# Kernel tuning notes

Measured on AMD Instinct MI355X. Metric: run time of the kernel, lower is better.

Reference implementation:

```python
import jax, jax.numpy as jnp
import numpy as np

B, S, H = 8, 1024, 1024
NH, HD = 16, 64
MBANK, TOPK = 128, 16
NLAYERS, FF = 12, 4096
EPS = 1e-5


def _ln(x, w, b):
    m = x.mean(-1, keepdims=True)
    v = ((x - m) ** 2).mean(-1, keepdims=True)
    return (x - m) / jnp.sqrt(v + EPS) * w + b


def _split_heads(x):  # [B,S,H] -> [B,NH,S,HD]
    return x.reshape(B, S, NH, HD).transpose(0, 2, 1, 3)


def _sdpa(q, k, v):  # inputs [B,NH,S,HD]
    scores = jnp.einsum('bhqd,bhkd->bhqk', q, k) / jnp.sqrt(jnp.float32(HD))
    attn = jax.nn.softmax(scores, axis=-1)
    o = jnp.einsum('bhqk,bhkd->bhqd', attn, v)
    return o.transpose(0, 2, 1, 3).reshape(B, S, H)


def setup_inputs() -> dict:
    key = jax.random.key(0)
    ks = jax.random.split(key, 24)
    n = lambda k, shp, s=0.02: jax.random.normal(k, shp, jnp.float32) * s
    return {
        'hidden_states': jax.random.normal(ks[0], (B, S, H), jnp.float32),
        'ln1_w': jnp.ones((H,), jnp.float32), 'ln1_b': jnp.zeros((H,), jnp.float32),
        'ln2_w': jnp.ones((H,), jnp.float32), 'ln2_b': jnp.zeros((H,), jnp.float32),
        'rec_wq': n(ks[1], (H, H)), 'rec_wk': n(ks[2], (H, H)),
        'rec_wv': n(ks[3], (H, H)), 'rec_wo': n(ks[4], (H, H)),
        'rec_ad_w1': n(ks[5], (H // 4, H)), 'rec_ad_w2': n(ks[6], (H, H // 4)),
        'mem_bank': n(ks[7], (MBANK, H)),
        'alloc_w': n(ks[8], (MBANK, H)), 'alloc_b': jnp.zeros((MBANK,), jnp.float32),
        'retr_w': n(ks[9], (MBANK, H)), 'retr_b': jnp.zeros((MBANK,), jnp.float32),
        'upd_w': n(ks[10], (H, H)), 'upd_b': jnp.zeros((H,), jnp.float32),
        'mem_scales': jnp.full((NLAYERS,), 0.1, jnp.float32),
        'attn_in_w': n(ks[11], (3 * H, H)), 'attn_in_b': jnp.zeros((3 * H,), jnp.float32),
        'attn_out_w': n(ks[12], (H, H)), 'attn_out_b': jnp.zeros((H,), jnp.float32),
        'mlp_w1': n(ks[13], (FF, H)), 'mlp_b1': jnp.zeros((FF,), jnp.float32),
        'mlp_w2': n(ks[14], (H, FF)), 'mlp_b2': jnp.zeros((H,), jnp.float32),
        'layer_idx': 4,
    }


def reference(hidden_states, ln1_w, ln1_b, ln2_w, ln2_b,
              rec_wq, rec_wk, rec_wv, rec_wo, rec_ad_w1, rec_ad_w2,
              mem_bank, alloc_w, alloc_b, retr_w, retr_b, upd_w, upd_b, mem_scales,
              attn_in_w, attn_in_b, attn_out_w, attn_out_b,
              mlp_w1, mlp_b1, mlp_w2, mlp_b2, layer_idx):
    residual = hidden_states
    h = _ln(hidden_states, ln1_w, ln1_b)

    # --- CrossLayerParameterRecycler (layer_idx % 4 == 0 and > 0 -> recycle) ---
    if layer_idx % 4 == 0 and layer_idx > 0:
        q = _split_heads(h @ rec_wq.T)
        k = _split_heads(h @ rec_wk.T)
        v = _split_heads(h @ rec_wv.T)
        base_out = _sdpa(q, k, v) @ rec_wo.T
        h = jax.nn.relu(base_out @ rec_ad_w1.T) @ rec_ad_w2.T

    # --- CrossLayerMemoryManager ---
    pooled = h.mean(axis=1)                                  # [B,H]
    alloc_weights = jax.nn.softmax(pooled @ alloc_w.T + alloc_b, axis=-1)   # [B,MBANK]
    retr_weights = jax.nn.softmax(pooled @ retr_w.T + retr_b, axis=-1)
    retrieved = retr_weights @ mem_bank                      # [B,H]
    h = h + retrieved[:, None, :] * mem_scales[layer_idx]
    update_signals = jax.nn.sigmoid(h.mean(axis=1) @ upd_w.T + upd_b)       # [B,H]
    _, top_idx = jax.lax.top_k(alloc_weights, TOPK)          # [B,TOPK]

    # sequential per-batch scatter (later batches overwrite earlier, as in torch loop)
    def _write(mb, be):
        idx, sig = be
        return mb.at[idx].set(jnp.broadcast_to(sig, (TOPK, H))), None
    new_mem_bank, _ = jax.lax.scan(_write, mem_bank, (top_idx, update_signals))

    # --- self attention (nn.MultiheadAttention, batch_first) ---
    qkv = h @ attn_in_w.T + attn_in_b                        # [B,S,3H]
    q, k, v = jnp.split(qkv, 3, axis=-1)
    attn_out = _sdpa(_split_heads(q), _split_heads(k), _split_heads(v))
    attn_out = attn_out @ attn_out_w.T + attn_out_b
    h = residual + attn_out

    # --- MLP block ---
    residual2 = h
    h = _ln(h, ln2_w, ln2_b)
    h = jax.nn.gelu(h @ mlp_w1.T + mlp_b1, approximate=False) @ mlp_w2.T + mlp_b2
    out = residual2 + h
    return out, new_mem_bank
```

## Files before the change

kernel.cpp:

```cpp
#include <hip/hip_runtime.h>
#include <hip/hip_bf16.h>
#include <math.h>
#include <stdint.h>


#define BB 8
#define SS 1024
#define HH 1024
#define NHEAD 16
#define HD 64
#define MBANK 128
#define TOPK_N 16
#define FF_DIM 4096
#define MROWS (BB * SS)
#define NB_ELEM (8ull*1024*1024)

typedef __bf16 bf16x8 __attribute__((ext_vector_type(8)));
typedef __bf16 bf16x4 __attribute__((ext_vector_type(4)));
typedef float f32x4 __attribute__((ext_vector_type(4)));

#define SCALE_LOG2E 0.18033688011112042f

__device__ __forceinline__ unsigned short f2b(float x) {
  unsigned u = __float_as_uint(x);
  unsigned r = (u + 0x7FFFu + ((u >> 16) & 1u)) >> 16;
  return (unsigned short)r;
}
__device__ __forceinline__ float b2f(unsigned short u) {
  return __uint_as_float((unsigned)u << 16);
}

__device__ __forceinline__ float hmax4(f32x4 v) {
  return fmaxf(fmaxf(v[0], v[1]), fmaxf(v[2], v[3]));
}

__device__ __forceinline__ void load16_lds(const void* g, void* lds_base, int lane) {
#if __has_builtin(__builtin_amdgcn_global_load_lds)
  typedef const __attribute__((address_space(1))) unsigned int guint;
  typedef __attribute__((address_space(3))) unsigned int luint;
  __builtin_amdgcn_global_load_lds((guint*)(uintptr_t)g,
                                   (luint*)(unsigned long long)(unsigned int)(uintptr_t)lds_base,
                                   16, 0, 0);
#else
  *(uint4*)((char*)lds_base + lane * 16) = *(const uint4*)g;
#endif
}

__device__ __forceinline__ float gelu_exact(float x) {
  return 0.5f * x * (1.f + erff(x * 0.70710678118654752440f));
}


__global__ __launch_bounds__(256) void cast_split(const float* __restrict__ s,
                                                  unsigned short* __restrict__ hi,
                                                  unsigned short* __restrict__ lo, int n4) {
  int i = blockIdx.x * 256 + threadIdx.x;
  if (i < n4) {
    float4 v = ((const float4*)s)[i];
    ushort4 h, l;
    h.x = f2b(v.x); l.x = f2b(v.x - b2f(h.x));
    h.y = f2b(v.y); l.y = f2b(v.y - b2f(h.y));
    h.z = f2b(v.z); l.z = f2b(v.z - b2f(h.z));
    h.w = f2b(v.w); l.w = f2b(v.w - b2f(h.w));
    ((ushort4*)hi)[i] = h;
    ((ushort4*)lo)[i] = l;
  }
}

__global__ __launch_bounds__(256) void ln3(const float* __restrict__ x,
                                           const float* __restrict__ w,
                                           const float* __restrict__ b,
                                           unsigned short* __restrict__ yh,
                                           unsigned short* __restrict__ yl) {
  int row = blockIdx.x;
  const float* xr = x + (size_t)row * HH;
  int t = threadIdx.x;
  float v[4];
  float s = 0.f, ss = 0.f;
#pragma unroll
  for (int i = 0; i < 4; i++) {
    v[i] = xr[t + i * 256];
    s += v[i];
    ss += v[i] * v[i];
  }
  __shared__ float rs[8], rss[8];
  for (int o = 32; o > 0; o >>= 1) {
    s += __shfl_down(s, o, 64);
    ss += __shfl_down(ss, o, 64);
  }
  int wid = t >> 6, lane = t & 63;
  if (lane == 0) { rs[wid] = s; rss[wid] = ss; }
  __syncthreads();
  if (t == 0) {
    float S = rs[0] + rs[1] + rs[2] + rs[3];
    float SSum = rss[0] + rss[1] + rss[2] + rss[3];
    float m = S * (1.f / HH);
    float var = SSum * (1.f / HH) - m * m;
    rs[4] = m;
    rs[5] = rsqrtf(var + 1e-5f);
  }
  __syncthreads();
  float m = rs[4], inv = rs[5];
#pragma unroll
  for (int i = 0; i < 4; i++) {
    int c = t + i * 256;
    float y = (v[i] - m) * inv * w[c] + b[c];
    unsigned short h = f2b(y);
    yh[(size_t)row * HH + c] = h;
    yl[(size_t)row * HH + c] = f2b(y - b2f(h));
  }
}

template <int ACT, int MODE>
__global__ __launch_bounds__(256) void gemm3(const unsigned short* __restrict__ Ah,
                                             const unsigned short* __restrict__ Al, int lda,
                                             const unsigned short* __restrict__ Wh,
                                             const unsigned short* __restrict__ Wl, int ldw,
                                             unsigned short* __restrict__ Oh,
                                             unsigned short* __restrict__ Ol,
                                             float* __restrict__ outF,
                                             int ldo, int K) {
  __shared__ unsigned short Ash[2][128 * 32];
  __shared__ unsigned short Asl[2][128 * 32];
  __shared__ unsigned short Bsh[2][128 * 32];
  __shared__ unsigned short Bsl[2][128 * 32];
  int n0 = blockIdx.x * 128, m0 = blockIdx.y * 128;
  int t = threadIdx.x, w = t >> 6, L = t & 63, quad = L >> 4, l16 = L & 15;
  int wm = w & 1, wn = w >> 1;
  const f32x4 vzero = {0.f, 0.f, 0.f, 0.f};
  f32x4 acc[4][4];
#pragma unroll
  for (int i = 0; i < 4; i++)
#pragma unroll
    for (int j = 0; j < 4; j++) acc[i][j] = vzero;
  int srow = L >> 2;
  int scol = ((L & 3) ^ ((L >> 3) & 3)) * 8;
  int rsw = (l16 >> 1) & 3;

  auto stage = [&](int buf, int k0) {
#pragma unroll
    for (int c = 0; c < 2; c++) {
      int r = (c * 4 + w) * 16 + srow;
      size_t aoff = (size_t)(m0 + r) * lda + k0 + scol;
      size_t boff = (size_t)(n0 + r) * ldw + k0 + scol;
      load16_lds(Ah + aoff, &Ash[buf][(c * 4 + w) * 512], L);
      load16_lds(Al + aoff, &Asl[buf][(c * 4 + w) * 512], L);
      load16_lds(Wh + boff, &Bsh[buf][(c * 4 + w) * 512], L);
      load16_lds(Wl + boff, &Bsl[buf][(c * 4 + w) * 512], L);
    }
  };
  auto compute = [&](int buf) {
    bf16x8 afh[4], afl[4], bfh[4], bfl[4];
#pragma unroll
    for (int i = 0; i < 4; i++) {
      int off = (wm * 64 + i * 16 + l16) * 32 + (quad ^ rsw) * 8;
      afh[i] = *(const bf16x8*)&Ash[buf][off];
      afl[i] = *(const bf16x8*)&Asl[buf][off];
    }
#pragma unroll
    for (int j = 0; j < 4; j++) {
      int off = (wn * 64 + j * 16 + l16) * 32 + (quad ^ rsw) * 8;
      bfh[j] = *(const bf16x8*)&Bsh[buf][off];
      bfl[j] = *(const bf16x8*)&Bsl[buf][off];
    }
#pragma unroll
    for (int i = 0; i < 4; i++)
#pragma unroll
      for (int j = 0; j < 4; j++) {
        acc[i][j] = __builtin_amdgcn_mfma_f32_16x16x32_bf16(afh[i], bfh[j], acc[i][j], 0, 0, 0);
        acc[i][j] = __builtin_amdgcn_mfma_f32_16x16x32_bf16(afh[i], bfl[j], acc[i][j], 0, 0, 0);
        acc[i][j] = __builtin_amdgcn_mfma_f32_16x16x32_bf16(afl[i], bfh[j], acc[i][j], 0, 0, 0);
      }
  };

  stage(0, 0);
  __syncthreads();
  for (int k0 = 0; k0 < K; k0 += 64) {
    stage(1, k0 + 32);
    compute(0);
    __syncthreads();
    if (k0 + 64 < K) stage(0, k0 + 64);
    compute(1);
    __syncthreads();
  }
#pragma unroll
  for (int i = 0; i < 4; i++) {
    int mb = m0 + wm * 64 + i * 16 + quad * 4;
#pragma unroll
    for (int j = 0; j < 4; j++) {
      int n = n0 + wn * 64 + j * 16 + l16;
      if (MODE == 1) {
        ushort4 sh, sl;
        float vv[4];
#pragma unroll
        for (int r = 0; r < 4; r++) {
          float v = acc[i][j][r];
          if (ACT == 1) v = fmaxf(v, 0.f);
          vv[r] = v;
        }
        sh.x = f2b(vv[0]); sl.x = f2b(vv[0] - b2f(sh.x));
        sh.y = f2b(vv[1]); sl.y = f2b(vv[1] - b2f(sh.y));
        sh.z = f2b(vv[2]); sl.z = f2b(vv[2] - b2f(sh.z));
        sh.w = f2b(vv[3]); sl.w = f2b(vv[3] - b2f(sh.w));
        *(ushort4*)&Oh[(size_t)n * ldo + mb] = sh;
        *(ushort4*)&Ol[(size_t)n * ldo + mb] = sl;
      } else {
#pragma unroll
        for (int r = 0; r < 4; r++) {
          float v = acc[i][j][r];
          if (ACT == 1) v = fmaxf(v, 0.f);
          size_t off = (size_t)(mb + r) * ldo + n;
          if (MODE == 0) {
            unsigned short h = f2b(v);
            Oh[off] = h;
            Ol[off] = f2b(v - b2f(h));
          } else {
            outF[off] = v;
          }
        }
      }
    }
  }
}

__global__ __launch_bounds__(256) void sdpa3(const unsigned short* __restrict__ Qh,
                                             const unsigned short* __restrict__ Ql,
                                             const unsigned short* __restrict__ Kh,
                                             const unsigned short* __restrict__ Kl,
                                             const unsigned short* __restrict__ Vth,
                                             const unsigned short* __restrict__ Vtl,
                                             unsigned short* __restrict__ Oh,
                                             unsigned short* __restrict__ Ol) {
  __shared__ unsigned short Ksh[64 * 64];
  __shared__ unsigned short Ksl[64 * 64];
  __shared__ unsigned short Vsh[64 * 64];
  __shared__ unsigned short Vsl[64 * 64];
  int qt = blockIdx.x, h = blockIdx.y, b = blockIdx.z;
  int t = threadIdx.x, w = t >> 6, L = t & 63, quad = L >> 4, l16 = L & 15;
  int q0 = qt * 64;
  const f32x4 vzero = {0.f, 0.f, 0.f, 0.f};
  bf16x8 qfh[2], qfl[2];
  {
    size_t qrow = (size_t)(b * SS + q0 + w * 16 + l16);
#pragma unroll
    for (int kh = 0; kh < 2; kh++) {
      size_t off = qrow * HH + h * 64 + kh * 32 + quad * 8;
      qfh[kh] = *(const bf16x8*)&Qh[off];
      qfl[kh] = *(const bf16x8*)&Ql[off];
    }
  }
  float mprev = -1e30f, lsum = 0.f;
  f32x4 oacc[4];
#pragma unroll
  for (int jd = 0; jd < 4; jd++) oacc[jd] = vzero;
  int srow = L >> 3;
  int scolV = ((L & 7) ^ srow) * 8;
  int rbase = ((l16 & 12) << 1) | (l16 & 3);
  int keyK = (l16 & 3) | (((l16 >> 2) & 1) << 2);
  int k7 = l16 & 7;
  for (int k0 = 0; k0 < SS; k0 += 64) {
    __syncthreads();
#pragma unroll
    for (int c = 0; c < 2; c++) {
      int rr = (c * 4 + w) * 8 + srow;
      int scolK = ((L & 7) ^ ((srow & 3) | (((c * 4 + w) & 1) << 2))) * 8;
      size_t koff = (size_t)(b * SS + k0 + rr) * HH + h * 64 + scolK;
      size_t voff = (size_t)(h * 64 + rr) * MROWS + b * SS + k0 + scolV;
      load16_lds(Kh + koff, &Ksh[(c * 4 + w) * 512], L);
      load16_lds(Kl + koff, &Ksl[(c * 4 + w) * 512], L);
      load16_lds(Vth + voff, &Vsh[(c * 4 + w) * 512], L);
      load16_lds(Vtl + voff, &Vsl[(c * 4 + w) * 512], L);
    }
    __syncthreads();
    f32x4 sacc[4];
#pragma unroll
    for (int jn = 0; jn < 4; jn++) sacc[jn] = vzero;
#pragma unroll
    for (int jn = 0; jn < 4; jn++) {
      int rowp = rbase + (jn & 1) * 4 + (jn >> 1) * 32;
#pragma unroll
      for (int kh = 0; kh < 2; kh++) {
        int off = rowp * 64 + (((kh * 4 + quad) ^ keyK) << 3);
        bf16x8 kfh = *(const bf16x8*)&Ksh[off];
        bf16x8 kfl = *(const bf16x8*)&Ksl[off];
        sacc[jn] = __builtin_amdgcn_mfma_f32_16x16x32_bf16(kfh, qfh[kh], sacc[jn], 0, 0, 0);
        sacc[jn] = __builtin_amdgcn_mfma_f32_16x16x32_bf16(kfl, qfh[kh], sacc[jn], 0, 0, 0);
        sacc[jn] = __builtin_amdgcn_mfma_f32_16x16x32_bf16(kfh, qfl[kh], sacc[jn], 0, 0, 0);
      }
    }
    float mt = fmaxf(fmaxf(hmax4(sacc[0]), hmax4(sacc[1])),
                     fmaxf(hmax4(sacc[2]), hmax4(sacc[3])));
    mt = fmaxf(mt, __shfl_xor(mt, 16, 64));
    mt = fmaxf(mt, __shfl_xor(mt, 32, 64));
    float m2 = fmaxf(mprev, mt * SCALE_LOG2E);
    float alpha = exp2f(mprev - m2);
    mprev = m2;
    float rs = 0.f;
    bf16x8 pah[2], pal[2];
#pragma unroll
    for (int jn = 0; jn < 4; jn++) {
      int kh = jn >> 1, half = (jn & 1) * 4;
#pragma unroll
      for (int r = 0; r < 4; r++) {
        float p = exp2f(fmaf(sacc[jn][r], SCALE_LOG2E, -m2));
        rs += p;
        __bf16 ph = (__bf16)p;
        pah[kh][half + r] = ph;
        pal[kh][half + r] = (__bf16)(p - (float)ph);
      }
    }
    rs += __shfl_xor(rs, 16, 64);
    rs += __shfl_xor(rs, 32, 64);
    lsum = lsum * alpha + rs;
    float ar[4];
#pragma unroll
    for (int r = 0; r < 4; r++) ar[r] = __shfl(alpha, quad * 4 + r, 16);
#pragma unroll
    for (int jd = 0; jd < 4; jd++)
#pragma unroll
      for (int r = 0; r < 4; r++) oacc[jd][r] *= ar[r];
#pragma unroll
    for (int jd = 0; jd < 4; jd++)
#pragma unroll
      for (int kh = 0; kh < 2; kh++) {
        int off = (jd * 16 + l16) * 64 + ((kh * 4 + quad) ^ k7) * 8;
        bf16x8 vfh = *(const bf16x8*)&Vsh[off];
        bf16x8 vfl = *(const bf16x8*)&Vsl[off];
        oacc[jd] = __builtin_amdgcn_mfma_f32_16x16x32_bf16(pah[kh], vfh, oacc[jd], 0, 0, 0);
        oacc[jd] = __builtin_amdgcn_mfma_f32_16x16x32_bf16(pah[kh], vfl, oacc[jd], 0, 0, 0);
        oacc[jd] = __builtin_amdgcn_mfma_f32_16x16x32_bf16(pal[kh], vfh, oacc[jd], 0, 0, 0);
      }
  }
  float inv = 1.f / lsum;
  float invr[4];
#pragma unroll
  for (int r = 0; r < 4; r++) invr[r] = __shfl(inv, quad * 4 + r, 16);
#pragma unroll
  for (int r = 0; r < 4; r++) {
    size_t row = (size_t)(b * SS + q0 + w * 16 + quad * 4 + r);
#pragma unroll
    for (int jd = 0; jd < 4; jd++) {
      float v = oacc[jd][r] * invr[r];
      unsigned short hh = f2b(v);
      size_t off = row * HH + h * 64 + jd * 16 + l16;
      Oh[off] = hh;
      Ol[off] = f2b(v - b2f(hh));
    }
  }
}


__global__ __launch_bounds__(256) void meanpool_kernel(const float* __restrict__ Hb,
                                                       float* __restrict__ P) {
  int cb = blockIdx.x;
  int b = blockIdx.y;
  int t = threadIdx.x;
  int c = (t & 63) + cb * 64;
  int part = t >> 6;
  float s = 0.f;
  const float* p = Hb + ((size_t)b * SS + part * 256) * HH + c;
  for (int j = 0; j < 256; j++) s += p[(size_t)j * HH];
  __shared__ float red[4][64];
  red[part][t & 63] = s;
  __syncthreads();
  if (t < 64) {
    float tot = red[0][t] + red[1][t] + red[2][t] + red[3][t];
    P[b * HH + cb * 64 + t] = tot * (1.f / SS);
  }
}

__global__ __launch_bounds__(256) void memlogits_kernel(const float* __restrict__ P,
                                                        const float* __restrict__ AW,
                                                        const float* __restrict__ ABias,
                                                        const float* __restrict__ RW,
                                                        const float* __restrict__ RBias,
                                                        float* __restrict__ LA,
                                                        float* __restrict__ LR) {
  int m = blockIdx.x, b = blockIdx.y;
  int t = threadIdx.x;
  const float* pr = P + b * HH;
  const float* aw = AW + (size_t)m * HH;
  const float* rw = RW + (size_t)m * HH;
  float sa = 0.f, sr = 0.f;
  for (int i = t; i < HH; i += 256) {
    float pv = pr[i];
    sa = fmaf(pv, aw[i], sa);
    sr = fmaf(pv, rw[i], sr);
  }
  for (int o = 32; o > 0; o >>= 1) {
    sa += __shfl_down(sa, o, 64);
    sr += __shfl_down(sr, o, 64);
  }
  __shared__ float ra[4], rr[4];
  if ((t & 63) == 0) { ra[t >> 6] = sa; rr[t >> 6] = sr; }
  __syncthreads();
  if (t == 0) {
    LA[b * MBANK + m] = ra[0] + ra[1] + ra[2] + ra[3] + ABias[m];
    LR[b * MBANK + m] = rr[0] + rr[1] + rr[2] + rr[3] + RBias[m];
  }
}

__global__ __launch_bounds__(256) void retrieve_kernel(const float* __restrict__ LA,
                                                       const float* __restrict__ LR,
                                                       const float* __restrict__ MB,
                                                       float* __restrict__ RET,
                                                       int* __restrict__ ISTOP) {
  int b = blockIdx.x;
  int t = threadIdx.x;
  __shared__ float rw[MBANK];
  __shared__ float la[MBANK];
  if (t < MBANK) {
    la[t] = LA[b * MBANK + t];
    rw[t] = LR[b * MBANK + t];
  }
  __syncthreads();
  if (t == 0) {
    float mx = -1e30f;
    for (int i = 0; i < MBANK; i++) mx = fmaxf(mx, rw[i]);
    float s = 0.f;
    for (int i = 0; i < MBANK; i++) {
      float e = __expf(rw[i] - mx);
      rw[i] = e;
      s += e;
    }
    float inv = 1.f / s;
    for (int i = 0; i < MBANK; i++) rw[i] *= inv;
  }
  __syncthreads();
  if (t < MBANK) {
    float mine = la[t];
    int rank = 0;
    for (int i = 0; i < MBANK; i++) {
      float o = la[i];
      if (o > mine || (o == mine && i < t)) rank++;
    }
    ISTOP[b * MBANK + t] = (rank < TOPK_N) ? 1 : 0;
  }
  for (int c = t; c < HH; c += 256) {
    float s = 0.f;
    for (int m = 0; m < MBANK; m++) s = fmaf(rw[m], MB[(size_t)m * HH + c], s);
    RET[b * HH + c] = s;
  }
}

__global__ __launch_bounds__(256) void addmem_kernel(float* __restrict__ Hb,
                                                     const float* __restrict__ RET,
                                                     const float* __restrict__ scales,
                                                     const int* __restrict__ lidx) {
  float sc = scales[lidx[0]];
  size_t i = (size_t)blockIdx.x * 256 + threadIdx.x;
  int c = (int)(i & 1023);
  int b = (int)(i >> 20);
  Hb[i] = fmaf(RET[b * HH + c], sc, Hb[i]);
}

__global__ __launch_bounds__(256) void upd_kernel(const float* __restrict__ P2,
                                                  const float* __restrict__ UW,
                                                  const float* __restrict__ UB,
                                                  float* __restrict__ UPD) {
  int n = blockIdx.x, b = blockIdx.y;
  int t = threadIdx.x;
  const float* pr = P2 + b * HH;
  const float* wr = UW + (size_t)n * HH;
  float s = 0.f;
  for (int i = t; i < HH; i += 256) s = fmaf(pr[i], wr[i], s);
  for (int o = 32; o > 0; o >>= 1) s += __shfl_down(s, o, 64);
  __shared__ float red[4];
  if ((t & 63) == 0) red[t >> 6] = s;
  __syncthreads();
  if (t == 0) {
    float tot = red[0] + red[1] + red[2] + red[3] + UB[n];
    UPD[b * HH + n] = 1.f / (1.f + __expf(-tot));
  }
}

__global__ __launch_bounds__(256) void membank_kernel(const float* __restrict__ MB,
                                                      const int* __restrict__ ISTOP,
                                                      const float* __restrict__ UPD,
                                                      float* __restrict__ OUT) {
  int row = blockIdx.x;
  int col = blockIdx.y * 256 + threadIdx.x;
  int w = -1;
  for (int b = 0; b < BB; b++)
    if (ISTOP[b * MBANK + row]) w = b;
  float v = (w >= 0) ? UPD[w * HH + col] : MB[(size_t)row * HH + col];
  OUT[(size_t)row * HH + col] = v;
}


__global__ __launch_bounds__(256) void ln_bf(const float* __restrict__ x,
                                             const float* __restrict__ w,
                                             const float* __restrict__ b,
                                             unsigned short* __restrict__ y) {
  int row = blockIdx.x;
  const float* xr = x + (size_t)row * HH;
  unsigned short* yr = y + (size_t)row * HH;
  int t = threadIdx.x;
  float v[4];
  float s = 0.f, ss = 0.f;
#pragma unroll
  for (int i = 0; i < 4; i++) {
    v[i] = xr[t + i * 256];
    s += v[i];
    ss += v[i] * v[i];
  }
  __shared__ float rs[8], rss[8];
  for (int o = 32; o > 0; o >>= 1) {
    s += __shfl_down(s, o, 64);
    ss += __shfl_down(ss, o, 64);
  }
  int wid = t >> 6, lane = t & 63;
  if (lane == 0) { rs[wid] = s; rss[wid] = ss; }
  __syncthreads();
  if (t == 0) {
    float S = rs[0] + rs[1] + rs[2] + rs[3];
    float SSum = rss[0] + rss[1] + rss[2] + rss[3];
    float m = S * (1.f / HH);
    float var = SSum * (1.f / HH) - m * m;
    rs[4] = m;
    rs[5] = rsqrtf(var + 1e-5f);
  }
  __syncthreads();
  float m = rs[4], inv = rs[5];
#pragma unroll
  for (int i = 0; i < 4; i++) {
    int c = t + i * 256;
    yr[c] = f2b((v[i] - m) * inv * w[c] + b[c]);
  }
}

__global__ __launch_bounds__(256) void castf2b(const float* __restrict__ s,
                                               unsigned short* __restrict__ d, int n4) {
  int i = blockIdx.x * 256 + threadIdx.x;
  if (i < n4) {
    float4 v = ((const float4*)s)[i];
    ushort4 o;
    o.x = f2b(v.x); o.y = f2b(v.y); o.z = f2b(v.z); o.w = f2b(v.w);
    ((ushort4*)d)[i] = o;
  }
}

template <int ACT, int MODE>
__global__ __launch_bounds__(256) void gemm_bf(const unsigned short* __restrict__ A, int lda,
                                               const unsigned short* __restrict__ W, int ldw,
                                               const float* __restrict__ bias,
                                               const float* __restrict__ resid,
                                               float* __restrict__ outF,
                                               unsigned short* __restrict__ outB,
                                               int ldo, int K) {
  __shared__ unsigned short As[2][128 * 32];
  __shared__ unsigned short Bs[2][128 * 32];
  int n0 = blockIdx.x * 128, m0 = blockIdx.y * 128;
  int t = threadIdx.x, w = t >> 6, L = t & 63, quad = L >> 4, l16 = L & 15;
  int wm = w & 1, wn = w >> 1;
  const f32x4 vzero = {0.f, 0.f, 0.f, 0.f};
  f32x4 acc[4][4];
#pragma unroll
  for (int i = 0; i < 4; i++)
#pragma unroll
    for (int j = 0; j < 4; j++) acc[i][j] = vzero;
  int srow = L >> 2;
  int scol = ((L & 3) ^ ((L >> 3) & 3)) * 8;
  int rsw = (l16 >> 1) & 3;

  auto stage = [&](int buf, int k0) {
#pragma unroll
    for (int c = 0; c < 2; c++) {
      int r = (c * 4 + w) * 16 + srow;
      load16_lds(A + (size_t)(m0 + r) * lda + k0 + scol, &As[buf][(c * 4 + w) * 512], L);
      load16_lds(W + (size_t)(n0 + r) * ldw + k0 + scol, &Bs[buf][(c * 4 + w) * 512], L);
    }
  };
  auto compute = [&](int buf) {
    bf16x8 af[4], bfr[4];
#pragma unroll
    for (int i = 0; i < 4; i++)
      af[i] = *(const bf16x8*)&As[buf][(wm * 64 + i * 16 + l16) * 32 + (quad ^ rsw) * 8];
#pragma unroll
    for (int j = 0; j < 4; j++)
      bfr[j] = *(const bf16x8*)&Bs[buf][(wn * 64 + j * 16 + l16) * 32 + (quad ^ rsw) * 8];
#pragma unroll
    for (int i = 0; i < 4; i++)
#pragma unroll
      for (int j = 0; j < 4; j++)
        acc[i][j] = __builtin_amdgcn_mfma_f32_16x16x32_bf16(af[i], bfr[j], acc[i][j], 0, 0, 0);
  };

  stage(0, 0);
  __syncthreads();
  for (int k0 = 0; k0 < K; k0 += 64) {
    stage(1, k0 + 32);
    compute(0);
    __syncthreads();
    if (k0 + 64 < K) stage(0, k0 + 64);
    compute(1);
    __syncthreads();
  }
#pragma unroll
  for (int i = 0; i < 4; i++) {
    int mb = m0 + wm * 64 + i * 16 + quad * 4;
#pragma unroll
    for (int j = 0; j < 4; j++) {
      int n = n0 + wn * 64 + j * 16 + l16;
      float bv = bias ? bias[n] : 0.f;
      if (MODE == 2) {
        ushort4 st;
        float v0 = acc[i][j][0] + bv, v1 = acc[i][j][1] + bv;
        float v2 = acc[i][j][2] + bv, v3 = acc[i][j][3] + bv;
        if (ACT == 1) { v0 = fmaxf(v0, 0.f); v1 = fmaxf(v1, 0.f); v2 = fmaxf(v2, 0.f); v3 = fmaxf(v3, 0.f); }
        if (ACT == 2) { v0 = gelu_exact(v0); v1 = gelu_exact(v1); v2 = gelu_exact(v2); v3 = gelu_exact(v3); }
        st.x = f2b(v0); st.y = f2b(v1); st.z = f2b(v2); st.w = f2b(v3);
        *(ushort4*)&outB[(size_t)n * ldo + mb] = st;
      } else {
#pragma unroll
        for (int r = 0; r < 4; r++) {
          float v = acc[i][j][r] + bv;
          if (ACT == 1) v = fmaxf(v, 0.f);
          if (ACT == 2) v = gelu_exact(v);
          size_t off = (size_t)(mb + r) * ldo + n;
          if (MODE == 1) outB[off] = f2b(v);
          else if (MODE == 3) outF[off] += v;
          else if (MODE == 4) outF[off] = v + resid[off];
        }
      }
    }
  }
}

__global__ __launch_bounds__(256) void sdpa_bf(const unsigned short* __restrict__ Q,
                                               const unsigned short* __restrict__ Kb,
                                               const unsigned short* __restrict__ Vt,
                                               unsigned short* __restrict__ O) {
  __shared__ unsigned short Ks[64 * 64];
  __shared__ unsigned short Vs[64 * 64];
  int qt = blockIdx.x, h = blockIdx.y, b = blockIdx.z;
  int t = threadIdx.x, w = t >> 6, L = t & 63, quad = L >> 4, l16 = L & 15;
  int q0 = qt * 64;
  const f32x4 vzero = {0.f, 0.f, 0.f, 0.f};
  bf16x8 qf[2];
  {
    size_t qrow = (size_t)(b * SS + q0 + w * 16 + l16);
#pragma unroll
    for (int kh = 0; kh < 2; kh++)
      qf[kh] = *(const bf16x8*)&Q[qrow * HH + h * 64 + kh * 32 + quad * 8];
  }
  float mprev = -1e30f, lsum = 0.f;
  f32x4 oacc[4];
#pragma unroll
  for (int jd = 0; jd < 4; jd++) oacc[jd] = vzero;
  int srow = L >> 3;
  int scolV = ((L & 7) ^ srow) * 8;
  int rbase = ((l16 & 12) << 1) | (l16 & 3);
  int keyK = (l16 & 3) | (((l16 >> 2) & 1) << 2);
  int k7 = l16 & 7;
  for (int k0 = 0; k0 < SS; k0 += 64) {
    __syncthreads();
#pragma unroll
    for (int c = 0; c < 2; c++) {
      int rr = (c * 4 + w) * 8 + srow;
      int scolK = ((L & 7) ^ ((srow & 3) | (((c * 4 + w) & 1) << 2))) * 8;
      load16_lds(Kb + (size_t)(b * SS + k0 + rr) * HH + h * 64 + scolK, &Ks[(c * 4 + w) * 512], L);
      load16_lds(Vt + (size_t)(h * 64 + rr) * MROWS + b * SS + k0 + scolV, &Vs[(c * 4 + w) * 512], L);
    }
    __syncthreads();
    f32x4 sacc[4];
#pragma unroll
    for (int jn = 0; jn < 4; jn++) sacc[jn] = vzero;
#pragma unroll
    for (int jn = 0; jn < 4; jn++) {
      int rowp = rbase + (jn & 1) * 4 + (jn >> 1) * 32;
#pragma unroll
      for (int kh = 0; kh < 2; kh++) {
        bf16x8 kf = *(const bf16x8*)&Ks[rowp * 64 + (((kh * 4 + quad) ^ keyK) << 3)];
        sacc[jn] = __builtin_amdgcn_mfma_f32_16x16x32_bf16(kf, qf[kh], sacc[jn], 0, 0, 0);
      }
    }
    float mt = fmaxf(fmaxf(hmax4(sacc[0]), hmax4(sacc[1])),
                     fmaxf(hmax4(sacc[2]), hmax4(sacc[3])));
    mt = fmaxf(mt, __shfl_xor(mt, 16, 64));
    mt = fmaxf(mt, __shfl_xor(mt, 32, 64));
    float m2 = fmaxf(mprev, mt * SCALE_LOG2E);
    float alpha = exp2f(mprev - m2);
    mprev = m2;
    float rs = 0.f;
    bf16x8 pa[2];
#pragma unroll
    for (int jn = 0; jn < 4; jn++) {
      int kh = jn >> 1, half = (jn & 1) * 4;
#pragma unroll
      for (int r = 0; r < 4; r++) {
        float p = exp2f(fmaf(sacc[jn][r], SCALE_LOG2E, -m2));
        rs += p;
        pa[kh][half + r] = (__bf16)p;
      }
    }
    rs += __shfl_xor(rs, 16, 64);
    rs += __shfl_xor(rs, 32, 64);
    lsum = lsum * alpha + rs;
    float ar[4];
#pragma unroll
    for (int r = 0; r < 4; r++) ar[r] = __shfl(alpha, quad * 4 + r, 16);
#pragma unroll
    for (int jd = 0; jd < 4; jd++)
#pragma unroll
      for (int r = 0; r < 4; r++) oacc[jd][r] *= ar[r];
#pragma unroll
    for (int jd = 0; jd < 4; jd++)
#pragma unroll
      for (int kh = 0; kh < 2; kh++) {
        bf16x8 vf = *(const bf16x8*)&Vs[(jd * 16 + l16) * 64 + ((kh * 4 + quad) ^ k7) * 8];
        oacc[jd] = __builtin_amdgcn_mfma_f32_16x16x32_bf16(pa[kh], vf, oacc[jd], 0, 0, 0);
      }
  }
  float inv = 1.f / lsum;
  float invr[4];
#pragma unroll
  for (int r = 0; r < 4; r++) invr[r] = __shfl(inv, quad * 4 + r, 16);
#pragma unroll
  for (int r = 0; r < 4; r++) {
    size_t row = (size_t)(b * SS + q0 + w * 16 + quad * 4 + r);
#pragma unroll
    for (int jd = 0; jd < 4; jd++)
      O[row * HH + h * 64 + jd * 16 + l16] = f2b(oacc[jd][r] * invr[r]);
  }
}

extern "C" void kernel_launch(void* const* d_in, const int* in_sizes, int n_in,
                              void* d_out, int out_size, void* d_ws, size_t ws_size,
                              hipStream_t stream) {
  const float* x = (const float*)d_in[0];
  const float* ln1_w = (const float*)d_in[1];
  const float* ln1_b = (const float*)d_in[2];
  const float* ln2_w = (const float*)d_in[3];
  const float* ln2_b = (const float*)d_in[4];
  const float* rec_wq = (const float*)d_in[5];
  const float* rec_wk = (const float*)d_in[6];
  const float* rec_wv = (const float*)d_in[7];
  const float* rec_wo = (const float*)d_in[8];
  const float* rec_ad_w1 = (const float*)d_in[9];
  const float* rec_ad_w2 = (const float*)d_in[10];
  const float* mem_bank = (const float*)d_in[11];
  const float* alloc_w = (const float*)d_in[12];
  const float* alloc_b = (const float*)d_in[13];
  const float* retr_w = (const float*)d_in[14];
  const float* retr_b = (const float*)d_in[15];
  const float* upd_w = (const float*)d_in[16];
  const float* upd_b = (const float*)d_in[17];
  const float* mem_scales = (const float*)d_in[18];
  const float* attn_in_w = (const float*)d_in[19];
  const float* attn_in_b = (const float*)d_in[20];
  const float* attn_out_w = (const float*)d_in[21];
  const float* attn_out_b = (const float*)d_in[22];
  const float* mlp_w1 = (const float*)d_in[23];
  const float* mlp_b1 = (const float*)d_in[24];
  const float* mlp_w2 = (const float*)d_in[25];
  const float* mlp_b2 = (const float*)d_in[26];
  const int* layer_idx = (const int*)d_in[27];

  float* out = (float*)d_out;
  float* out_mb = out + NB_ELEM;

  const size_t U = NB_ELEM;
  unsigned short* W16 = (unsigned short*)d_ws;
  unsigned short* U0 = W16;
  unsigned short* U1 = W16 + U;
  unsigned short* U2 = W16 + 2 * U;
  unsigned short* U3 = W16 + 3 * U;
  unsigned short* U4 = W16 + 4 * U;
  unsigned short* U5 = W16 + 5 * U;
  unsigned short* wsh = W16 + 6 * U;
  unsigned short* wsl = wsh + 1048576;
  float* small = (float*)(wsl + 1048576);
  float* pooled = small;
  float* pooled2 = small + 8192;
  float* logitsA = small + 16384;
  float* logitsR = small + 17408;
  float* retrieved = small + 18432;
  float* updsig = small + 26624;
  int* istop = (int*)(small + 34816);
  unsigned short* D0 = (unsigned short*)out;
  unsigned short* D1 = D0 + U;
  unsigned short* ain_bf = U5;
  unsigned short* aout_bf = U5 + 3 * 1048576;

  dim3 blk(256);
  dim3 gG(8, 64);
  dim3 gG256(2, 64);
  dim3 gS(16, NHEAD, BB);
  const int EW_GRID = (int)(NB_ELEM / 256);

  ln3<<<MROWS, blk, 0, stream>>>(x, ln1_w, ln1_b, U0, U1);
  cast_split<<<1024, blk, 0, stream>>>(rec_wq, wsh, wsl, 262144);
  gemm3<0, 0><<<gG, blk, 0, stream>>>(U0, U1, HH, wsh, wsl, HH, U2, U3, nullptr, HH, HH);
  cast_split<<<1024, blk, 0, stream>>>(rec_wk, wsh, wsl, 262144);
  gemm3<0, 0><<<gG, blk, 0, stream>>>(U0, U1, HH, wsh, wsl, HH, U4, U5, nullptr, HH, HH);
  cast_split<<<1024, blk, 0, stream>>>(rec_wv, wsh, wsl, 262144);
  gemm3<0, 1><<<gG, blk, 0, stream>>>(U0, U1, HH, wsh, wsl, HH, D0, D1, nullptr, MROWS, HH);
  sdpa3<<<gS, blk, 0, stream>>>(U2, U3, U4, U5, D0, D1, U0, U1);
  cast_split<<<1024, blk, 0, stream>>>(rec_wo, wsh, wsl, 262144);
  gemm3<0, 0><<<gG, blk, 0, stream>>>(U0, U1, HH, wsh, wsl, HH, U2, U3, nullptr, HH, HH);
  cast_split<<<256, blk, 0, stream>>>(rec_ad_w1, wsh, wsl, 65536);
  gemm3<1, 0><<<gG256, blk, 0, stream>>>(U2, U3, HH, wsh, wsl, HH, U4, U4 + 2097152, nullptr, 256, HH);
  cast_split<<<256, blk, 0, stream>>>(rec_ad_w2, wsh, wsl, 65536);
  gemm3<0, 2><<<gG, blk, 0, stream>>>(U4, U4 + 2097152, 256, wsh, wsl, 256, nullptr, nullptr, out, HH, 256);
  meanpool_kernel<<<dim3(HH / 64, BB), blk, 0, stream>>>(out, pooled);
  memlogits_kernel<<<dim3(MBANK, BB), blk, 0, stream>>>(pooled, alloc_w, alloc_b, retr_w, retr_b, logitsA, logitsR);
  retrieve_kernel<<<BB, blk, 0, stream>>>(logitsA, logitsR, mem_bank, retrieved, istop);
  addmem_kernel<<<EW_GRID, blk, 0, stream>>>(out, retrieved, mem_scales, layer_idx);
  meanpool_kernel<<<dim3(HH / 64, BB), blk, 0, stream>>>(out, pooled2);
  upd_kernel<<<dim3(HH, BB), blk, 0, stream>>>(pooled2, upd_w, upd_b, updsig);
  membank_kernel<<<dim3(MBANK, HH / 256), blk, 0, stream>>>(mem_bank, istop, updsig, out_mb);
  castf2b<<<8192, blk, 0, stream>>>(out, U0, 2097152);
  castf2b<<<3072, blk, 0, stream>>>(attn_in_w, ain_bf, 786432);
  castf2b<<<1024, blk, 0, stream>>>(attn_out_w, aout_bf, 262144);
  gemm_bf<0, 1><<<gG, blk, 0, stream>>>(U0, HH, ain_bf, HH, attn_in_b, nullptr, nullptr, U1, HH, HH);
  gemm_bf<0, 1><<<gG, blk, 0, stream>>>(U0, HH, ain_bf + (size_t)HH * HH, HH, attn_in_b + HH, nullptr, nullptr, U2, HH, HH);
  gemm_bf<0, 2><<<gG, blk, 0, stream>>>(U0, HH, ain_bf + 2ull * HH * HH, HH, attn_in_b + 2 * HH, nullptr, nullptr, U3, MROWS, HH);
  sdpa_bf<<<gS, blk, 0, stream>>>(U1, U2, U3, U4);
  gemm_bf<0, 4><<<gG, blk, 0, stream>>>(U4, HH, aout_bf, HH, attn_out_b, x, out, nullptr, HH, HH);
  ln_bf<<<MROWS, blk, 0, stream>>>(out, ln2_w, ln2_b, U1);
  {
    unsigned short* w1b = U0;
    unsigned short* w2b = U0 + 4 * 1048576;
    unsigned short* h2 = U2;
    castf2b<<<4096, blk, 0, stream>>>(mlp_w1, w1b, 1048576);
    castf2b<<<4096, blk, 0, stream>>>(mlp_w2, w2b, 1048576);
    gemm_bf<2, 1><<<dim3(32, 64), blk, 0, stream>>>(U1, HH, w1b, HH, mlp_b1, nullptr, nullptr, h2, FF_DIM, HH);
    gemm_bf<0, 3><<<gG, blk, 0, stream>>>(h2, FF_DIM, w2b, FF_DIM, mlp_b2, nullptr, out, nullptr, HH, FF_DIM);
  }
}
```

Measured before the change: 1.136 ms.

## Double-buffer K/V tiles, swizzle block order, skip redundant rescale in attention

Both attention kernels now keep two K/V buffers in LDS and load the next 64-key tile while computing on the current one, halving the barriers per tile. The grid becomes 1-D, and the block index is remapped so blocks that run at the same time spread across XCDs while sharing batch and head data. The online-softmax rescale of the accumulator is skipped when no lane's running max changed. LDS use per block doubles, which may reduce occupancy, and the wave-level branch adds a small divergence check.

```diff
diff --git a/kernel.cpp b/kernel.cpp
--- a/kernel.cpp
+++ b/kernel.cpp
@@ -231,11 +231,13 @@
                                              const unsigned short* __restrict__ Vtl,
                                              unsigned short* __restrict__ Oh,
                                              unsigned short* __restrict__ Ol) {
-  __shared__ unsigned short Ksh[64 * 64];
-  __shared__ unsigned short Ksl[64 * 64];
-  __shared__ unsigned short Vsh[64 * 64];
-  __shared__ unsigned short Vsl[64 * 64];
-  int qt = blockIdx.x, h = blockIdx.y, b = blockIdx.z;
+  __shared__ unsigned short Ksh[2][64 * 64];
+  __shared__ unsigned short Ksl[2][64 * 64];
+  __shared__ unsigned short Vsh[2][64 * 64];
+  __shared__ unsigned short Vsl[2][64 * 64];
+  int wg = (int)blockIdx.x;
+  int swz = (wg & 7) * 256 + (wg >> 3);
+  int qt = swz & 15, h = (swz >> 4) & 15, b = swz >> 8;
   int t = threadIdx.x, w = t >> 6, L = t & 63, quad = L >> 4, l16 = L & 15;
   int q0 = qt * 64;
   const f32x4 vzero = {0.f, 0.f, 0.f, 0.f};
@@ -258,20 +260,22 @@
   int rbase = ((l16 & 12) << 1) | (l16 & 3);
   int keyK = (l16 & 3) | (((l16 >> 2) & 1) << 2);
   int k7 = l16 & 7;
-  for (int k0 = 0; k0 < SS; k0 += 64) {
-    __syncthreads();
+
+  auto stage = [&](int buf, int k0) {
 #pragma unroll
     for (int c = 0; c < 2; c++) {
       int rr = (c * 4 + w) * 8 + srow;
       int scolK = ((L & 7) ^ ((srow & 3) | (((c * 4 + w) & 1) << 2))) * 8;
       size_t koff = (size_t)(b * SS + k0 + rr) * HH + h * 64 + scolK;
       size_t voff = (size_t)(h * 64 + rr) * MROWS + b * SS + k0 + scolV;
-      load16_lds(Kh + koff, &Ksh[(c * 4 + w) * 512], L);
-      load16_lds(Kl + koff, &Ksl[(c * 4 + w) * 512], L);
-      load16_lds(Vth + voff, &Vsh[(c * 4 + w) * 512], L);
-      load16_lds(Vtl + voff, &Vsl[(c * 4 + w) * 512], L);
-    }
-    __syncthreads();
+      load16_lds(Kh + koff, &Ksh[buf][(c * 4 + w) * 512], L);
+      load16_lds(Kl + koff, &Ksl[buf][(c * 4 + w) * 512], L);
+      load16_lds(Vth + voff, &Vsh[buf][(c * 4 + w) * 512], L);
+      load16_lds(Vtl + voff, &Vsl[buf][(c * 4 + w) * 512], L);
+    }
+  };
+
+  auto computeTile = [&](int buf) {
     f32x4 sacc[4];
 #pragma unroll
     for (int jn = 0; jn < 4; jn++) sacc[jn] = vzero;
@@ -281,8 +285,8 @@
 #pragma unroll
       for (int kh = 0; kh < 2; kh++) {
         int off = rowp * 64 + (((kh * 4 + quad) ^ keyK) << 3);
-        bf16x8 kfh = *(const bf16x8*)&Ksh[off];
-        bf16x8 kfl = *(const bf16x8*)&Ksl[off];
+        bf16x8 kfh = *(const bf16x8*)&Ksh[buf][off];
+        bf16x8 kfl = *(const bf16x8*)&Ksl[buf][off];
         sacc[jn] = __builtin_amdgcn_mfma_f32_16x16x32_bf16(kfh, qfh[kh], sacc[jn], 0, 0, 0);
         sacc[jn] = __builtin_amdgcn_mfma_f32_16x16x32_bf16(kfl, qfh[kh], sacc[jn], 0, 0, 0);
         sacc[jn] = __builtin_amdgcn_mfma_f32_16x16x32_bf16(kfh, qfl[kh], sacc[jn], 0, 0, 0);
@@ -293,8 +297,6 @@
     mt = fmaxf(mt, __shfl_xor(mt, 16, 64));
     mt = fmaxf(mt, __shfl_xor(mt, 32, 64));
     float m2 = fmaxf(mprev, mt * SCALE_LOG2E);
-    float alpha = exp2f(mprev - m2);
-    mprev = m2;
     float rs = 0.f;
     bf16x8 pah[2], pal[2];
 #pragma unroll
@@ -311,25 +313,42 @@
     }
     rs += __shfl_xor(rs, 16, 64);
     rs += __shfl_xor(rs, 32, 64);
-    lsum = lsum * alpha + rs;
-    float ar[4];
-#pragma unroll
-    for (int r = 0; r < 4; r++) ar[r] = __shfl(alpha, quad * 4 + r, 16);
-#pragma unroll
-    for (int jd = 0; jd < 4; jd++)
-#pragma unroll
-      for (int r = 0; r < 4; r++) oacc[jd][r] *= ar[r];
+    if (__any(m2 != mprev)) {
+      float alpha = exp2f(mprev - m2);
+      lsum = lsum * alpha + rs;
+      float ar[4];
+#pragma unroll
+      for (int r = 0; r < 4; r++) ar[r] = __shfl(alpha, quad * 4 + r, 16);
+#pragma unroll
+      for (int jd = 0; jd < 4; jd++)
+#pragma unroll
+        for (int r = 0; r < 4; r++) oacc[jd][r] *= ar[r];
+    } else {
+      lsum += rs;
+    }
+    mprev = m2;
 #pragma unroll
     for (int jd = 0; jd < 4; jd++)
 #pragma unroll
       for (int kh = 0; kh < 2; kh++) {
         int off = (jd * 16 + l16) * 64 + ((kh * 4 + quad) ^ k7) * 8;
-        bf16x8 vfh = *(const bf16x8*)&Vsh[off];
-        bf16x8 vfl = *(const bf16x8*)&Vsl[off];
+        bf16x8 vfh = *(const bf16x8*)&Vsh[buf][off];
+        bf16x8 vfl = *(const bf16x8*)&Vsl[buf][off];
         oacc[jd] = __builtin_amdgcn_mfma_f32_16x16x32_bf16(pah[kh], vfh, oacc[jd], 0, 0, 0);
         oacc[jd] = __builtin_amdgcn_mfma_f32_16x16x32_bf16(pah[kh], vfl, oacc[jd], 0, 0, 0);
         oacc[jd] = __builtin_amdgcn_mfma_f32_16x16x32_bf16(pal[kh], vfh, oacc[jd], 0, 0, 0);
       }
+  };
+
+  stage(0, 0);
+  __syncthreads();
+  for (int k0 = 0; k0 < SS; k0 += 128) {
+    stage(1, k0 + 64);
+    computeTile(0);
+    __syncthreads();
+    if (k0 + 128 < SS) stage(0, k0 + 128);
+    computeTile(1);
+    __syncthreads();
   }
   float inv = 1.f / lsum;
   float invr[4];
@@ -631,9 +650,11 @@
                                                const unsigned short* __restrict__ Kb,
                                                const unsigned short* __restrict__ Vt,
                                                unsigned short* __restrict__ O) {
-  __shared__ unsigned short Ks[64 * 64];
-  __shared__ unsigned short Vs[64 * 64];
-  int qt = blockIdx.x, h = blockIdx.y, b = blockIdx.z;
+  __shared__ unsigned short Ks[2][64 * 64];
+  __shared__ unsigned short Vs[2][64 * 64];
+  int wg = (int)blockIdx.x;
+  int swz = (wg & 7) * 256 + (wg >> 3);
+  int qt = swz & 15, h = (swz >> 4) & 15, b = swz >> 8;
   int t = threadIdx.x, w = t >> 6, L = t & 63, quad = L >> 4, l16 = L & 15;
   int q0 = qt * 64;
   const f32x4 vzero = {0.f, 0.f, 0.f, 0.f};
@@ -653,16 +674,18 @@
   int rbase = ((l16 & 12) << 1) | (l16 & 3);
   int keyK = (l16 & 3) | (((l16 >> 2) & 1) << 2);
   int k7 = l16 & 7;
-  for (int k0 = 0; k0 < SS; k0 += 64) {
-    __syncthreads();
+
+  auto stage = [&](int buf, int k0) {
 #pragma unroll
     for (int c = 0; c < 2; c++) {
       int rr = (c * 4 + w) * 8 + srow;
       int scolK = ((L & 7) ^ ((srow & 3) | (((c * 4 + w) & 1) << 2))) * 8;
-      load16_lds(Kb + (size_t)(b * SS + k0 + rr) * HH + h * 64 + scolK, &Ks[(c * 4 + w) * 512], L);
-      load16_lds(Vt + (size_t)(h * 64 + rr) * MROWS + b * SS + k0 + scolV, &Vs[(c * 4 + w) * 512], L);
-    }
-    __syncthreads();
+      load16_lds(Kb + (size_t)(b * SS + k0 + rr) * HH + h * 64 + scolK, &Ks[buf][(c * 4 + w) * 512], L);
+      load16_lds(Vt + (size_t)(h * 64 + rr) * MROWS + b * SS + k0 + scolV, &Vs[buf][(c * 4 + w) * 512], L);
+    }
+  };
+
+  auto computeTile = [&](int buf) {
     f32x4 sacc[4];
 #pragma unroll
     for (int jn = 0; jn < 4; jn++) sacc[jn] = vzero;
@@ -671,7 +694,7 @@
       int rowp = rbase + (jn & 1) * 4 + (jn >> 1) * 32;
 #pragma unroll
       for (int kh = 0; kh < 2; kh++) {
-        bf16x8 kf = *(const bf16x8*)&Ks[rowp * 64 + (((kh * 4 + quad) ^ keyK) << 3)];
+        bf16x8 kf = *(const bf16x8*)&Ks[buf][rowp * 64 + (((kh * 4 + quad) ^ keyK) << 3)];
         sacc[jn] = __builtin_amdgcn_mfma_f32_16x16x32_bf16(kf, qf[kh], sacc[jn], 0, 0, 0);
       }
     }
@@ -680,8 +703,6 @@
     mt = fmaxf(mt, __shfl_xor(mt, 16, 64));
     mt = fmaxf(mt, __shfl_xor(mt, 32, 64));
     float m2 = fmaxf(mprev, mt * SCALE_LOG2E);
-    float alpha = exp2f(mprev - m2);
-    mprev = m2;
     float rs = 0.f;
     bf16x8 pa[2];
 #pragma unroll
@@ -696,21 +717,38 @@
     }
     rs += __shfl_xor(rs, 16, 64);
     rs += __shfl_xor(rs, 32, 64);
-    lsum = lsum * alpha + rs;
-    float ar[4];
-#pragma unroll
-    for (int r = 0; r < 4; r++) ar[r] = __shfl(alpha, quad * 4 + r, 16);
+    if (__any(m2 != mprev)) {
+      float alpha = exp2f(mprev - m2);
+      lsum = lsum * alpha + rs;
+      float ar[4];
+#pragma unroll
+      for (int r = 0; r < 4; r++) ar[r] = __shfl(alpha, quad * 4 + r, 16);
+#pragma unroll
+      for (int jd = 0; jd < 4; jd++)
+#pragma unroll
+        for (int r = 0; r < 4; r++) oacc[jd][r] *= ar[r];
+    } else {
+      lsum += rs;
+    }
+    mprev = m2;
 #pragma unroll
     for (int jd = 0; jd < 4; jd++)
 #pragma unroll
-      for (int r = 0; r < 4; r++) oacc[jd][r] *= ar[r];
-#pragma unroll
-    for (int jd = 0; jd < 4; jd++)
-#pragma unroll
       for (int kh = 0; kh < 2; kh++) {
-        bf16x8 vf = *(const bf16x8*)&Vs[(jd * 16 + l16) * 64 + ((kh * 4 + quad) ^ k7) * 8];
+        bf16x8 vf = *(const bf16x8*)&Vs[buf][(jd * 16 + l16) * 64 + ((kh * 4 + quad) ^ k7) * 8];
         oacc[jd] = __builtin_amdgcn_mfma_f32_16x16x32_bf16(pa[kh], vf, oacc[jd], 0, 0, 0);
       }
+  };
+
+  stage(0, 0);
+  __syncthreads();
+  for (int k0 = 0; k0 < SS; k0 += 128) {
+    stage(1, k0 + 64);
+    computeTile(0);
+    __syncthreads();
+    if (k0 + 128 < SS) stage(0, k0 + 128);
+    computeTile(1);
+    __syncthreads();
   }
   float inv = 1.f / lsum;
   float invr[4];
@@ -786,7 +824,7 @@
   dim3 blk(256);
   dim3 gG(8, 64);
   dim3 gG256(2, 64);
-  dim3 gS(16, NHEAD, BB);
+  dim3 gS1(2048);
   const int EW_GRID = (int)(NB_ELEM / 256);
 
   ln3<<<MROWS, blk, 0, stream>>>(x, ln1_w, ln1_b, U0, U1);
@@ -796,7 +834,7 @@
   gemm3<0, 0><<<gG, blk, 0, stream>>>(U0, U1, HH, wsh, wsl, HH, U4, U5, nullptr, HH, HH);
   cast_split<<<1024, blk, 0, stream>>>(rec_wv, wsh, wsl, 262144);
   gemm3<0, 1><<<gG, blk, 0, stream>>>(U0, U1, HH, wsh, wsl, HH, D0, D1, nullptr, MROWS, HH);
-  sdpa3<<<gS, blk, 0, stream>>>(U2, U3, U4, U5, D0, D1, U0, U1);
+  sdpa3<<<gS1, blk, 0, stream>>>(U2, U3, U4, U5, D0, D1, U0, U1);
   cast_split<<<1024, blk, 0, stream>>>(rec_wo, wsh, wsl, 262144);
   gemm3<0, 0><<<gG, blk, 0, stream>>>(U0, U1, HH, wsh, wsl, HH, U2, U3, nullptr, HH, HH);
   cast_split<<<256, blk, 0, stream>>>(rec_ad_w1, wsh, wsl, 65536);
@@ -816,7 +854,7 @@
   gemm_bf<0, 1><<<gG, blk, 0, stream>>>(U0, HH, ain_bf, HH, attn_in_b, nullptr, nullptr, U1, HH, HH);
   gemm_bf<0, 1><<<gG, blk, 0, stream>>>(U0, HH, ain_bf + (size_t)HH * HH, HH, attn_in_b + HH, nullptr, nullptr, U2, HH, HH);
   gemm_bf<0, 2><<<gG, blk, 0, stream>>>(U0, HH, ain_bf + 2ull * HH * HH, HH, attn_in_b + 2 * HH, nullptr, nullptr, U3, MROWS, HH);
-  sdpa_bf<<<gS, blk, 0, stream>>>(U1, U2, U3, U4);
+  sdpa_bf<<<gS1, blk, 0, stream>>>(U1, U2, U3, U4);
   gemm_bf<0, 4><<<gG, blk, 0, stream>>>(U4, HH, aout_bf, HH, attn_out_b, x, out, nullptr, HH, HH);
   ln_bf<<<MROWS, blk, 0, stream>>>(out, ln2_w, ln2_b, U1);
   {
```

Result: no change. 1.153 ms (+1.5%).

## Read V directly from global, swizzle attention grid, skip redundant rescale

Applied to the files above, without the earlier changes.

Both attention kernels stop staging V tiles in shared memory and read V fragments straight from global memory into registers, which cuts LDS traffic and footprint. The 3D grid becomes a 1D grid with an XCD-aware swizzle, so blocks sharing a (batch, head) land on the same chiplet and can reuse K/V in its L2. The online-softmax rescale of the accumulators is skipped when no row's running max changed in the wavefront. Each V row segment is now fetched separately by every wave, so performance depends on cache hits and may lose the coalescing the LDS staging gave.

```diff
diff --git a/kernel.cpp b/kernel.cpp
--- a/kernel.cpp
+++ b/kernel.cpp
@@ -233,9 +233,9 @@
                                              unsigned short* __restrict__ Ol) {
   __shared__ unsigned short Ksh[64 * 64];
   __shared__ unsigned short Ksl[64 * 64];
-  __shared__ unsigned short Vsh[64 * 64];
-  __shared__ unsigned short Vsl[64 * 64];
-  int qt = blockIdx.x, h = blockIdx.y, b = blockIdx.z;
+  int wg = (int)blockIdx.x;
+  int swz = (wg & 7) * 256 + (wg >> 3);
+  int qt = swz & 15, h = (swz >> 4) & 15, b = swz >> 8;
   int t = threadIdx.x, w = t >> 6, L = t & 63, quad = L >> 4, l16 = L & 15;
   int q0 = qt * 64;
   const f32x4 vzero = {0.f, 0.f, 0.f, 0.f};
@@ -254,10 +254,11 @@
 #pragma unroll
   for (int jd = 0; jd < 4; jd++) oacc[jd] = vzero;
   int srow = L >> 3;
-  int scolV = ((L & 7) ^ srow) * 8;
   int rbase = ((l16 & 12) << 1) | (l16 & 3);
   int keyK = (l16 & 3) | (((l16 >> 2) & 1) << 2);
-  int k7 = l16 & 7;
+  const unsigned short* Vbh = Vth + (size_t)(h * 64 + l16) * MROWS + b * SS + quad * 8;
+  const unsigned short* Vbl = Vtl + (size_t)(h * 64 + l16) * MROWS + b * SS + quad * 8;
+
   for (int k0 = 0; k0 < SS; k0 += 64) {
     __syncthreads();
 #pragma unroll
@@ -265,11 +266,8 @@
       int rr = (c * 4 + w) * 8 + srow;
       int scolK = ((L & 7) ^ ((srow & 3) | (((c * 4 + w) & 1) << 2))) * 8;
       size_t koff = (size_t)(b * SS + k0 + rr) * HH + h * 64 + scolK;
-      size_t voff = (size_t)(h * 64 + rr) * MROWS + b * SS + k0 + scolV;
       load16_lds(Kh + koff, &Ksh[(c * 4 + w) * 512], L);
       load16_lds(Kl + koff, &Ksl[(c * 4 + w) * 512], L);
-      load16_lds(Vth + voff, &Vsh[(c * 4 + w) * 512], L);
-      load16_lds(Vtl + voff, &Vsl[(c * 4 + w) * 512], L);
     }
     __syncthreads();
     f32x4 sacc[4];
@@ -293,8 +291,6 @@
     mt = fmaxf(mt, __shfl_xor(mt, 16, 64));
     mt = fmaxf(mt, __shfl_xor(mt, 32, 64));
     float m2 = fmaxf(mprev, mt * SCALE_LOG2E);
-    float alpha = exp2f(mprev - m2);
-    mprev = m2;
     float rs = 0.f;
     bf16x8 pah[2], pal[2];
 #pragma unroll
@@ -311,21 +307,27 @@
     }
     rs += __shfl_xor(rs, 16, 64);
     rs += __shfl_xor(rs, 32, 64);
-    lsum = lsum * alpha + rs;
-    float ar[4];
-#pragma unroll
-    for (int r = 0; r < 4; r++) ar[r] = __shfl(alpha, quad * 4 + r, 16);
+    if (__any(m2 != mprev)) {
+      float alpha = exp2f(mprev - m2);
+      lsum = lsum * alpha + rs;
+      float ar[4];
+#pragma unroll
+      for (int r = 0; r < 4; r++) ar[r] = __shfl(alpha, quad * 4 + r, 16);
+#pragma unroll
+      for (int jd = 0; jd < 4; jd++)
+#pragma unroll
+        for (int r = 0; r < 4; r++) oacc[jd][r] *= ar[r];
+    } else {
+      lsum += rs;
+    }
+    mprev = m2;
 #pragma unroll
     for (int jd = 0; jd < 4; jd++)
 #pragma unroll
-      for (int r = 0; r < 4; r++) oacc[jd][r] *= ar[r];
-#pragma unroll
-    for (int jd = 0; jd < 4; jd++)
-#pragma unroll
       for (int kh = 0; kh < 2; kh++) {
-        int off = (jd * 16 + l16) * 64 + ((kh * 4 + quad) ^ k7) * 8;
-        bf16x8 vfh = *(const bf16x8*)&Vsh[off];
-        bf16x8 vfl = *(const bf16x8*)&Vsl[off];
+        size_t voff = (size_t)(jd * 16) * MROWS + k0 + kh * 32;
+        bf16x8 vfh = *(const bf16x8*)&Vbh[voff];
+        bf16x8 vfl = *(const bf16x8*)&Vbl[voff];
         oacc[jd] = __builtin_amdgcn_mfma_f32_16x16x32_bf16(pah[kh], vfh, oacc[jd], 0, 0, 0);
         oacc[jd] = __builtin_amdgcn_mfma_f32_16x16x32_bf16(pah[kh], vfl, oacc[jd], 0, 0, 0);
         oacc[jd] = __builtin_amdgcn_mfma_f32_16x16x32_bf16(pal[kh], vfh, oacc[jd], 0, 0, 0);
@@ -632,8 +634,9 @@
                                                const unsigned short* __restrict__ Vt,
                                                unsigned short* __restrict__ O) {
   __shared__ unsigned short Ks[64 * 64];
-  __shared__ unsigned short Vs[64 * 64];
-  int qt = blockIdx.x, h = blockIdx.y, b = blockIdx.z;
+  int wg = (int)blockIdx.x;
+  int swz = (wg & 7) * 256 + (wg >> 3);
+  int qt = swz & 15, h = (swz >> 4) & 15, b = swz >> 8;
   int t = threadIdx.x, w = t >> 6, L = t & 63, quad = L >> 4, l16 = L & 15;
   int q0 = qt * 64;
   const f32x4 vzero = {0.f, 0.f, 0.f, 0.f};
@@ -649,10 +652,10 @@
 #pragma unroll
   for (int jd = 0; jd < 4; jd++) oacc[jd] = vzero;
   int srow = L >> 3;
-  int scolV = ((L & 7) ^ srow) * 8;
   int rbase = ((l16 & 12) << 1) | (l16 & 3);
   int keyK = (l16 & 3) | (((l16 >> 2) & 1) << 2);
-  int k7 = l16 & 7;
+  const unsigned short* Vb = Vt + (size_t)(h * 64 + l16) * MROWS + b * SS + quad * 8;
+
   for (int k0 = 0; k0 < SS; k0 += 64) {
     __syncthreads();
 #pragma unroll
@@ -660,7 +663,6 @@
       int rr = (c * 4 + w) * 8 + srow;
       int scolK = ((L & 7) ^ ((srow & 3) | (((c * 4 + w) & 1) << 2))) * 8;
       load16_lds(Kb + (size_t)(b * SS + k0 + rr) * HH + h * 64 + scolK, &Ks[(c * 4 + w) * 512], L);
-      load16_lds(Vt + (size_t)(h * 64 + rr) * MROWS + b * SS + k0 + scolV, &Vs[(c * 4 + w) * 512], L);
     }
     __syncthreads();
     f32x4 sacc[4];
@@ -680,8 +682,6 @@
     mt = fmaxf(mt, __shfl_xor(mt, 16, 64));
     mt = fmaxf(mt, __shfl_xor(mt, 32, 64));
     float m2 = fmaxf(mprev, mt * SCALE_LOG2E);
-    float alpha = exp2f(mprev - m2);
-    mprev = m2;
     float rs = 0.f;
     bf16x8 pa[2];
 #pragma unroll
@@ -696,19 +696,25 @@
     }
     rs += __shfl_xor(rs, 16, 64);
     rs += __shfl_xor(rs, 32, 64);
-    lsum = lsum * alpha + rs;
-    float ar[4];
-#pragma unroll
-    for (int r = 0; r < 4; r++) ar[r] = __shfl(alpha, quad * 4 + r, 16);
+    if (__any(m2 != mprev)) {
+      float alpha = exp2f(mprev - m2);
+      lsum = lsum * alpha + rs;
+      float ar[4];
+#pragma unroll
+      for (int r = 0; r < 4; r++) ar[r] = __shfl(alpha, quad * 4 + r, 16);
+#pragma unroll
+      for (int jd = 0; jd < 4; jd++)
+#pragma unroll
+        for (int r = 0; r < 4; r++) oacc[jd][r] *= ar[r];
+    } else {
+      lsum += rs;
+    }
+    mprev = m2;
 #pragma unroll
     for (int jd = 0; jd < 4; jd++)
 #pragma unroll
-      for (int r = 0; r < 4; r++) oacc[jd][r] *= ar[r];
-#pragma unroll
-    for (int jd = 0; jd < 4; jd++)
-#pragma unroll
       for (int kh = 0; kh < 2; kh++) {
-        bf16x8 vf = *(const bf16x8*)&Vs[(jd * 16 + l16) * 64 + ((kh * 4 + quad) ^ k7) * 8];
+        bf16x8 vf = *(const bf16x8*)&Vb[(size_t)(jd * 16) * MROWS + k0 + kh * 32];
         oacc[jd] = __builtin_amdgcn_mfma_f32_16x16x32_bf16(pa[kh], vf, oacc[jd], 0, 0, 0);
       }
   }
@@ -786,7 +792,7 @@
   dim3 blk(256);
   dim3 gG(8, 64);
   dim3 gG256(2, 64);
-  dim3 gS(16, NHEAD, BB);
+  dim3 gS1(2048);
   const int EW_GRID = (int)(NB_ELEM / 256);
 
   ln3<<<MROWS, blk, 0, stream>>>(x, ln1_w, ln1_b, U0, U1);
@@ -796,7 +802,7 @@
   gemm3<0, 0><<<gG, blk, 0, stream>>>(U0, U1, HH, wsh, wsl, HH, U4, U5, nullptr, HH, HH);
   cast_split<<<1024, blk, 0, stream>>>(rec_wv, wsh, wsl, 262144);
   gemm3<0, 1><<<gG, blk, 0, stream>>>(U0, U1, HH, wsh, wsl, HH, D0, D1, nullptr, MROWS, HH);
-  sdpa3<<<gS, blk, 0, stream>>>(U2, U3, U4, U5, D0, D1, U0, U1);
+  sdpa3<<<gS1, blk, 0, stream>>>(U2, U3, U4, U5, D0, D1, U0, U1);
   cast_split<<<1024, blk, 0, stream>>>(rec_wo, wsh, wsl, 262144);
   gemm3<0, 0><<<gG, blk, 0, stream>>>(U0, U1, HH, wsh, wsl, HH, U2, U3, nullptr, HH, HH);
   cast_split<<<256, blk, 0, stream>>>(rec_ad_w1, wsh, wsl, 65536);
@@ -816,7 +822,7 @@
   gemm_bf<0, 1><<<gG, blk, 0, stream>>>(U0, HH, ain_bf, HH, attn_in_b, nullptr, nullptr, U1, HH, HH);
   gemm_bf<0, 1><<<gG, blk, 0, stream>>>(U0, HH, ain_bf + (size_t)HH * HH, HH, attn_in_b + HH, nullptr, nullptr, U2, HH, HH);
   gemm_bf<0, 2><<<gG, blk, 0, stream>>>(U0, HH, ain_bf + 2ull * HH * HH, HH, attn_in_b + 2 * HH, nullptr, nullptr, U3, MROWS, HH);
-  sdpa_bf<<<gS, blk, 0, stream>>>(U1, U2, U3, U4);
+  sdpa_bf<<<gS1, blk, 0, stream>>>(U1, U2, U3, U4);
   gemm_bf<0, 4><<<gG, blk, 0, stream>>>(U4, HH, aout_bf, HH, attn_out_b, x, out, nullptr, HH, HH);
   ln_bf<<<MROWS, blk, 0, stream>>>(out, ln2_w, ln2_b, U1);
   {
```

Result: slower. 1.417 ms (+24.8%).
